# Kernel tuning notes

Measured on AMD Instinct MI355X. Metric: run time of the kernel, lower is better.

The kernel has to match this reference:

```python
import jax, jax.numpy as jnp
import numpy as np
import math

# ---------- real Clebsch-Gordan coupling tables (computed once, tiny) ----------
def _cg(j1, m1, j2, m2, j3, m3):
    if m1 + m2 != m3 or j3 < abs(j1 - j2) or j3 > j1 + j2:
        return 0.0
    f = math.factorial
    pre = ((2 * j3 + 1) * f(j3 + j1 - j2) * f(j3 - j1 + j2) * f(j1 + j2 - j3) / f(j1 + j2 + j3 + 1)) ** 0.5
    pre *= (f(j3 + m3) * f(j3 - m3) * f(j1 - m1) * f(j1 + m1) * f(j2 - m2) * f(j2 + m2)) ** 0.5
    s = 0.0
    for k in range(0, j1 + j2 - j3 + 1):
        d = (k, j1 + j2 - j3 - k, j1 - m1 - k, j2 + m2 - k, j3 - j2 + m1 + k, j3 - j1 - m2 + k)
        if min(d) < 0:
            continue
        den = 1
        for t in d:
            den *= f(t)
        s += (-1) ** k / den
    return pre * s

def _Q(l):  # complex->real spherical-harmonic change of basis
    Q = np.zeros((2 * l + 1, 2 * l + 1), dtype=complex)
    Q[l, l] = 1.0
    s = 2 ** -0.5
    for m in range(1, l + 1):
        Q[l + m, l + m] = (-1) ** m * s
        Q[l + m, l - m] = s
        Q[l - m, l + m] = -1j * (-1) ** m * s
        Q[l - m, l - m] = 1j * s
    return Q

def _K(l1, l2, l3):  # real coupling tensor [2l3+1, 2l1+1, 2l2+1]
    C = np.zeros((2 * l3 + 1, 2 * l1 + 1, 2 * l2 + 1), dtype=complex)
    for M3 in range(-l3, l3 + 1):
        for M1 in range(-l1, l1 + 1):
            for M2 in range(-l2, l2 + 1):
                C[M3 + l3, M1 + l1, M2 + l2] = _cg(l1, M1, l2, M2, l3, M3)
    K = np.einsum('cC,aA,bB,CAB->cab', _Q(l3).conj(), _Q(l1), _Q(l2), C)
    K = K.imag if np.abs(K.imag).max() > np.abs(K.real).max() else K.real
    return np.asarray(K, dtype=np.float32)

# the 9 'uvu' instructions (in_l, edge_l, out_l) with multiplicities (weight_numel=144)
_PATHS = [(0, 0, 0), (0, 2, 2), (1, 0, 1), (1, 2, 1), (1, 2, 2), (2, 0, 2), (2, 2, 0), (2, 2, 1), (2, 2, 2)]
_KT = [jnp.asarray(_K(*p)) for p in _PATHS]
_MULS = [32, 32, 16, 16, 16, 8, 8, 8, 8]
_SPLITS = np.cumsum(_MULS)[:-1].tolist()
NEI = 8
EPS = 1e-5

def _sh(u):  # component-normalized real SH of unit vectors, l=0..2 (m order -l..l, l=1 -> y,z,x)
    x, y, z = u[:, 0], u[:, 1], u[:, 2]
    sh0 = jnp.ones_like(x)[:, None]
    sh1 = np.float32(3 ** 0.5) * jnp.stack([y, z, x], -1)
    s15 = np.float32(15 ** 0.5)
    s5 = np.float32(5 ** 0.5)
    sh2 = jnp.stack([s15 * x * y, s15 * y * z, 0.5 * s5 * (3 * z * z - 1.0), s15 * x * z, 0.5 * s15 * (x * x - y * y)], -1)
    return sh0, sh1, sh2

def _path(xs, sh, wp, Kt):  # xs [E,u,2l1+1], sh [E,2l2+1], Kt [2l3+1,2l1+1,2l2+1] -> [E,u,2l3+1]
    return jnp.einsum('eui,ej,oij->euo', xs, sh, Kt) * wp[None, :, None]

def _layer(x0, x1, x2, pos, src, dst, w, W0, W1, W2, bw0, bb0, bw1, bw2, N):
    ev = pos[dst] - pos[src]
    u = ev / (jnp.linalg.norm(ev, axis=1, keepdims=True) + 1e-12)
    sh0, sh1, sh2 = _sh(u)
    s0 = x0[src][:, :, None]  # [E,32,1]
    s1 = x1[src]              # [E,16,3]
    s2 = x2[src]              # [E,8,5]
    ws = jnp.split(w, _SPLITS)
    p1 = _path(s0, sh0, ws[0], _KT[0])
    p2 = _path(s0, sh2, ws[1], _KT[1])
    p3 = _path(s1, sh0, ws[2], _KT[2])
    p4 = _path(s1, sh2, ws[3], _KT[3])
    p5 = _path(s1, sh2, ws[4], _KT[4])
    p6 = _path(s2, sh0, ws[5], _KT[5])
    p7 = _path(s2, sh2, ws[6], _KT[6])
    p8 = _path(s2, sh2, ws[7], _KT[7])
    p9 = _path(s2, sh2, ws[8], _KT[8])
    m0 = jnp.concatenate([p1, p7], 1)          # [E,40,1]
    m1 = jnp.concatenate([p3, p4, p8], 1)      # [E,40,3]
    m2 = jnp.concatenate([p2, p5, p6, p9], 1)  # [E,64,5]
    a0 = jax.ops.segment_sum(m0, dst, num_segments=N)
    a1 = jax.ops.segment_sum(m1, dst, num_segments=N)
    a2 = jax.ops.segment_sum(m2, dst, num_segments=N)
    y0 = (a0[:, :, 0] @ W0) * np.float32(1.0 / 40 ** 0.5)
    y1 = jnp.einsum('num,uv->nvm', a1, W1) * np.float32(1.0 / 40 ** 0.5)
    y2 = jnp.einsum('num,uv->nvm', a2, W2) * np.float32(1.0 / 64 ** 0.5)
    # equivariant batchnorm (training stats): scalars -> standard BN, l>0 -> norm BN
    f = y0 - y0.mean(0)
    y0 = f / jnp.sqrt((f * f).mean(0) + EPS) * bw0 + bb0
    y1 = y1 / jnp.sqrt((y1 * y1).mean(axis=(0, 2)) + EPS)[None, :, None] * bw1[None, :, None]
    y2 = y2 / jnp.sqrt((y2 * y2).mean(axis=(0, 2)) + EPS)[None, :, None] * bw2[None, :, None]
    return y0, y1, y2

def _forward(positions, W_emb, tp_w, lin_W0, lin_W1, lin_W2, bn_w0, bn_b0, bn_w1, bn_w2, Wf1, Wf2, bf2, Wf3, bf3):
    B, P, _ = positions.shape
    N = B * P
    pos = positions.reshape(N, 3)
    # kNN graph from dense cdist + topk (indices are not differentiated)
    pg = jax.lax.stop_gradient(pos)
    sq = jnp.sum(pg * pg, 1)
    d2 = sq[:, None] + sq[None, :] - 2.0 * (pg @ pg.T)
    _, idx = jax.lax.top_k(-d2, NEI + 1)  # smallest distances; col 0 is self
    src = jnp.repeat(jnp.arange(N), NEI)
    dst = idx[:, 1:].reshape(-1)
    x0 = jnp.ones((N, 1), jnp.float32) @ W_emb  # embedding: only 0e->0e path exists
    x1 = jnp.zeros((N, 16, 3), jnp.float32)
    x2 = jnp.zeros((N, 8, 5), jnp.float32)
    for l in range(3):
        y0, y1, y2 = _layer(x0, x1, x2, pos, src, dst, tp_w[l], lin_W0[l], lin_W1[l], lin_W2[l],
                            bn_w0[l], bn_b0[l], bn_w1[l], bn_w2[l], N)
        x0 = jax.nn.relu(y0) + x0
        x1 = jax.nn.relu(y1) + x1
        x2 = jax.nn.relu(y2) + x2
    h = jax.nn.relu((x0 @ Wf1) * np.float32(1.0 / 32 ** 0.5))  # scalar part -> 32x0e
    h = jax.nn.relu(h @ Wf2 + bf2)
    out = (h @ Wf3 + bf3).reshape(B, P, 2)
    return out

def setup_inputs() -> dict:
    key = jax.random.key(0)
    ks = jax.random.split(key, 16)
    B, P = 4, 2048
    return {
        'positions': jax.random.normal(ks[0], (B, P, 3), jnp.float32) * 3.0,
        'W_emb': jax.random.normal(ks[1], (1, 32), jnp.float32),
        'tp_w': jax.random.normal(ks[2], (3, 144), jnp.float32),
        'lin_W0': jax.random.normal(ks[3], (3, 40, 32), jnp.float32),
        'lin_W1': jax.random.normal(ks[4], (3, 40, 16), jnp.float32),
        'lin_W2': jax.random.normal(ks[5], (3, 64, 8), jnp.float32),
        'bn_w0': 1.0 + 0.05 * jax.random.normal(ks[6], (3, 32), jnp.float32),
        'bn_b0': jnp.zeros((3, 32), jnp.float32),
        'bn_w1': 1.0 + 0.05 * jax.random.normal(ks[7], (3, 16), jnp.float32),
        'bn_w2': 1.0 + 0.05 * jax.random.normal(ks[8], (3, 8), jnp.float32),
        'Wf1': jax.random.normal(ks[9], (32, 32), jnp.float32),
        'Wf2': jax.random.normal(ks[10], (32, 16), jnp.float32) * 0.2,
        'bf2': jax.random.normal(ks[11], (16,), jnp.float32) * 0.1,
        'Wf3': jax.random.normal(ks[12], (16, 2), jnp.float32) * 0.2,
        'bf3': jax.random.normal(ks[13], (2,), jnp.float32) * 0.1,
    }

def reference(positions, W_emb, tp_w, lin_W0, lin_W1, lin_W2, bn_w0, bn_b0, bn_w1, bn_w2, Wf1, Wf2, bf2, Wf3, bf3):
    return _forward(positions, W_emb, tp_w, lin_W0, lin_W1, lin_W2, bn_w0, bn_b0, bn_w1, bn_w2, Wf1, Wf2, bf2, Wf3, bf3)
```

## Files before the change

kernel.cpp:

```cpp
#include <hip/hip_runtime.h>
#include <math.h>

#define NN 8192
#define REV_CAP 48
#define KNN_CAP 512

static const size_t OFF_K     = 0;
static const size_t OFF_CNT   = 512;
static const size_t OFF_REV   = 8704;
static const size_t OFF_STATS = 401920;
static const size_t OFF_XF    = 406528;
static const size_t OFF_YF    = 1389568;
static const size_t WS_FLOATS = 2372608;

__device__ double dfact(int n){ double r=1.0; for(int i=2;i<=n;++i) r*=(double)i; return r; }

__device__ double dcg(int j1,int m1,int j2,int m2,int j3,int m3){
  if (m1+m2!=m3) return 0.0;
  if (j3 < abs(j1-j2) || j3 > j1+j2) return 0.0;
  double pre = sqrt((double)(2*j3+1)*dfact(j3+j1-j2)*dfact(j3-j1+j2)*dfact(j1+j2-j3)/dfact(j1+j2+j3+1));
  pre *= sqrt(dfact(j3+m3)*dfact(j3-m3)*dfact(j1-m1)*dfact(j1+m1)*dfact(j2-m2)*dfact(j2+m2));
  double s=0.0;
  for(int k=0;k<=j1+j2-j3;++k){
    int d1=j1+j2-j3-k, d2=j1-m1-k, d3=j2+m2-k, d4=j3-j2+m1+k, d5=j3-j1-m2+k;
    if(d1<0||d2<0||d3<0||d4<0||d5<0) continue;
    double den = dfact(k)*dfact(d1)*dfact(d2)*dfact(d3)*dfact(d4)*dfact(d5);
    s += ((k&1)? -1.0: 1.0)/den;
  }
  return pre*s;
}

__device__ int qrow(int l,int r,int* col,double* re,double* im){
  const double s = 0.70710678118654752440;
  if (r==l){ col[0]=l; re[0]=1.0; im[0]=0.0; return 1; }
  if (r>l){ int m=r-l;
    col[0]=l+m; re[0]=((m&1)?-s:s); im[0]=0.0;
    col[1]=l-m; re[1]=s;            im[1]=0.0;
  } else { int m=l-r;
    col[0]=l+m; re[0]=0.0; im[0]=((m&1)? s : -s);
    col[1]=l-m; re[1]=0.0; im[1]=s;
  }
  return 2;
}

__global__ __launch_bounds__(256) void k_setup(const float* __restrict__ pos,
        const float* __restrict__ W_emb, float* __restrict__ Kbuf,
        float* __restrict__ xf,
        float* __restrict__ xs, float* __restrict__ ys, float* __restrict__ zs,
        float* __restrict__ qs,
        int* __restrict__ cnt){
  int idx = blockIdx.x*256 + threadIdx.x;
  if (idx < 983040) { const int c = idx%120; xf[idx] = (c<32)? W_emb[c] : 0.f; return; }
  idx -= 983040;
  if (idx < 8192) {
    const float x=pos[3*idx], y=pos[3*idx+1], z=pos[3*idx+2];
    xs[idx]=x; ys[idx]=y; zs[idx]=z; qs[idx]=0.5f*(x*x+y*y+z*z);
    return;
  }
  idx -= 8192;
  if (idx < 8192) { cnt[idx]=0; return; }
  idx -= 8192;
  if (idx >= 405) return;

  const int tid = idx;
  const int sizes[9]={1,25,9,45,75,25,25,75,125};
  const int l1s[9]={0,0,1,1,1,2,2,2,2};
  const int l2s[9]={0,2,0,2,2,0,2,2,2};
  const int l3s[9]={0,2,1,1,2,2,0,1,2};
  int p=0, rem=tid;
  for(p=0;p<9;++p){ if(rem < sizes[p]) break; rem -= sizes[p]; }
  const int l1=l1s[p], l2=l2s[p], l3=l3s[p];
  const int n1=2*l1+1, n2=2*l2+1;
  const int c = rem/(n1*n2); const int r2 = rem%(n1*n2); const int a=r2/n2; const int b=r2%n2;

  int c3[2],c1[2],c2[2]; double re3[2],im3[2],re1[2],im1[2],re2[2],im2[2];
  const int nc3 = qrow(l3,c,c3,re3,im3);
  const int nc1 = qrow(l1,a,c1,re1,im1);
  const int nc2 = qrow(l2,b,c2,re2,im2);

  double accRe=0, accIm=0;
  for(int i3=0;i3<nc3;++i3){
    const double q3re=re3[i3], q3im=-im3[i3];
    for(int i1=0;i1<nc1;++i1){
      const double pre_re = q3re*re1[i1] - q3im*im1[i1];
      const double pre_im = q3re*im1[i1] + q3im*re1[i1];
      for(int i2=0;i2<nc2;++i2){
        const double cgv = dcg(l1, c1[i1]-l1, l2, c2[i2]-l2, l3, c3[i3]-l3);
        if (cgv==0.0) continue;
        accRe += (pre_re*re2[i2] - pre_im*im2[i2])*cgv;
        accIm += (pre_re*im2[i2] + pre_im*re2[i2])*cgv;
      }
    }
  }
  const bool useImag = ((l1+l2+l3)&1)!=0;
  Kbuf[tid] = (float)(useImag? accIm : accRe);
}

__global__ __launch_bounds__(256) void k_knn4(const float* __restrict__ xs,
                                              const float* __restrict__ ys,
                                              const float* __restrict__ zs,
                                              const float* __restrict__ qs,
                                              int* __restrict__ cnt, int* __restrict__ rev){
  const int lane = threadIdx.x & 63;
  const int w    = threadIdx.x >> 6;
  const int node = blockIdx.x*4 + w;
  __shared__ float sdist[4][KNN_CAP];
  __shared__ int   sidx[4][KNN_CAP];
  __shared__ int   scount[4];
  if (threadIdx.x < 4) scount[threadIdx.x]=0;
  __syncthreads();

  const float px = xs[node], py = ys[node], pz = zs[node];

  float m1 = INFINITY, m2 = INFINITY;
  for(int c=0;c<4;++c){
    const int base = (c*64 + lane)*4;
    const float4 fx = *(const float4*)(xs + base);
    const float4 fy = *(const float4*)(ys + base);
    const float4 fz = *(const float4*)(zs + base);
    const float4 fq = *(const float4*)(qs + base);
    float ss[4];
    ss[0] = fmaf(-px,fx.x, fmaf(-py,fy.x, fmaf(-pz,fz.x, fq.x)));
    ss[1] = fmaf(-px,fx.y, fmaf(-py,fy.y, fmaf(-pz,fz.y, fq.y)));
    ss[2] = fmaf(-px,fx.z, fmaf(-py,fy.z, fmaf(-pz,fz.z, fq.z)));
    ss[3] = fmaf(-px,fx.w, fmaf(-py,fy.w, fmaf(-pz,fz.w, fq.w)));
    #pragma unroll
    for(int q=0;q<4;++q){
      const float hi = fmaxf(m1, ss[q]);
      m1 = fminf(m1, ss[q]);
      m2 = fminf(m2, hi);
    }
  }
  float T = INFINITY;
  for(int r=0;r<9;++r){
    float v = m1; int l = lane;
    #pragma unroll
    for(int s=32;s>0;s>>=1){
      const float ov=__shfl_xor(v,s,64); const int ol=__shfl_xor(l,s,64);
      if (ov<v || (ov==v && ol<l)){ v=ov; l=ol; }
    }
    T = v;
    if (lane==l){ m1=m2; m2=INFINITY; }
  }

  for(int c=0;c<32;++c){
    const int base = (c*64 + lane)*4;
    const float4 fx = *(const float4*)(xs + base);
    const float4 fy = *(const float4*)(ys + base);
    const float4 fz = *(const float4*)(zs + base);
    const float4 fq = *(const float4*)(qs + base);
    float ss[4];
    ss[0] = fmaf(-px,fx.x, fmaf(-py,fy.x, fmaf(-pz,fz.x, fq.x)));
    ss[1] = fmaf(-px,fx.y, fmaf(-py,fy.y, fmaf(-pz,fz.y, fq.y)));
    ss[2] = fmaf(-px,fx.z, fmaf(-py,fy.z, fmaf(-pz,fz.z, fq.z)));
    ss[3] = fmaf(-px,fx.w, fmaf(-py,fy.w, fmaf(-pz,fz.w, fq.w)));
    #pragma unroll
    for(int q=0;q<4;++q){
      if (ss[q] <= T){
        int pos = atomicAdd(&scount[w],1);
        if (pos < KNN_CAP){ sdist[w][pos]=ss[q]; sidx[w][pos]=base+q; }
      }
    }
  }
  __syncthreads();

  int m = scount[w]; if (m > KNN_CAP) m = KNN_CAP;
  float dl[KNN_CAP/64]; int il[KNN_CAP/64];
  #pragma unroll
  for(int k=0;k<KNN_CAP/64;++k){
    const int j = lane + 64*k;
    if (j < m){ dl[k]=sdist[w][j]; il[k]=sidx[w][j]; }
    else      { dl[k]=INFINITY;    il[k]=0x7fffffff; }
  }
  for(int r=0;r<9;++r){
    float bv=dl[0]; int bi=il[0];
    #pragma unroll
    for(int k=1;k<KNN_CAP/64;++k){
      if (dl[k]<bv || (dl[k]==bv && il[k]<bi)){ bv=dl[k]; bi=il[k]; }
    }
    float v=bv; int ix=bi;
    #pragma unroll
    for(int s=32;s>0;s>>=1){
      float ov=__shfl_xor(v,s,64); int oi=__shfl_xor(ix,s,64);
      if (ov<v || (ov==v && oi<ix)){ v=ov; ix=oi; }
    }
    if (ix != node && lane==0){
      int cpos = atomicAdd(&cnt[ix],1);
      if (cpos < REV_CAP) rev[ix*REV_CAP + cpos] = node;
    }
    #pragma unroll
    for(int k=0;k<KNN_CAP/64;++k){
      if (il[k]==ix){ dl[k]=INFINITY; il[k]=0x7fffffff; }
    }
  }
}

__global__ __launch_bounds__(256) void k_msg(
  const float* __restrict__ pos,
  const int* __restrict__ cnt, const int* __restrict__ rev,
  const float* __restrict__ Kbuf,
  const float* __restrict__ xf,
  const float* __restrict__ tpw,
  const float* __restrict__ W0, const float* __restrict__ W1, const float* __restrict__ W2,
  float* __restrict__ yf)
{
  const int t = threadIdx.x;
  const int w = t >> 6;
  const int lane = t & 63;
  const int n = blockIdx.x*4 + w;

  __shared__ float KL[405];
  __shared__ float TW[144];
  __shared__ float momP[4][120];
  __shared__ float momS[4][600];
  __shared__ float aS[4][480];
  for(int q=t;q<405;q+=256) KL[q]=Kbuf[q];
  for(int q=t;q<144;q+=256) TW[q]=tpw[q];
  __syncthreads();

  const int deg0 = cnt[n];
  const int deg = (deg0<REV_CAP)? deg0 : REV_CAP;
  const float pnx=pos[3*n], pny=pos[3*n+1], pnz=pos[3*n+2];
  const int c0 = lane*2;
  float mp0=0.f, mp1=0.f;
  float ms0[5], ms1[5];
  #pragma unroll
  for(int j=0;j<5;++j){ ms0[j]=0.f; ms1[j]=0.f; }
  const float s15 = 3.8729833462f, s5c = 2.2360679775f;
  for(int e=0;e<deg;++e){
    const int i = rev[n*REV_CAP+e];
    const float ex = pnx - pos[3*i], ey = pny - pos[3*i+1], ez = pnz - pos[3*i+2];
    const float rn = sqrtf(ex*ex+ey*ey+ez*ez) + 1e-12f;
    const float ux=ex/rn, uy=ey/rn, uz=ez/rn;
    float sh[5];
    sh[0]=s15*ux*uy; sh[1]=s15*uy*uz; sh[2]=0.5f*s5c*(3.f*uz*uz-1.f);
    sh[3]=s15*ux*uz; sh[4]=0.5f*s15*(ux*ux-uy*uy);
    if (lane<60){
      const float2 f = *(const float2*)(xf + (size_t)i*120 + c0);
      mp0 += f.x; mp1 += f.y;
      ms0[0]+=f.x*sh[0]; ms0[1]+=f.x*sh[1]; ms0[2]+=f.x*sh[2]; ms0[3]+=f.x*sh[3]; ms0[4]+=f.x*sh[4];
      ms1[0]+=f.y*sh[0]; ms1[1]+=f.y*sh[1]; ms1[2]+=f.y*sh[2]; ms1[3]+=f.y*sh[3]; ms1[4]+=f.y*sh[4];
    }
  }
  if (lane<60){
    momP[w][c0]=mp0; momP[w][c0+1]=mp1;
    #pragma unroll
    for(int j=0;j<5;++j){ momS[w][c0*5+j]=ms0[j]; momS[w][(c0+1)*5+j]=ms1[j]; }
  }
  __syncthreads();

  float acc[14];
  #pragma unroll
  for(int k=0;k<14;++k) acc[k]=0.f;

  if (lane<32){
    const int u=lane;
    const float rw0=TW[u], rw1=TW[32+u];
    acc[0] = rw0 * KL[0] * momP[w][u];
    float m0s[5];
    #pragma unroll
    for(int j=0;j<5;++j) m0s[j]=momS[w][u*5+j];
    #pragma unroll
    for(int o=0;o<5;++o){ float g=0.f;
      #pragma unroll
      for(int j=0;j<5;++j) g += KL[1+o*5+j]*m0s[j];
      acc[1+o] = rw1*g; }
  } else if (lane<48){
    const int u=lane-32;
    const float rw0=TW[64+u], rw1=TW[80+u], rw2=TW[96+u];
    float m1p[3], m1s[3][5];
    #pragma unroll
    for(int i=0;i<3;++i){
      m1p[i]=momP[w][32+u*3+i];
      #pragma unroll
      for(int j=0;j<5;++j) m1s[i][j]=momS[w][(32+u*3+i)*5+j];
    }
    #pragma unroll
    for(int o=0;o<3;++o){ float g=0.f;
      #pragma unroll
      for(int i=0;i<3;++i) g += KL[26+o*3+i]*m1p[i];
      acc[o]=rw0*g; }
    #pragma unroll
    for(int o=0;o<3;++o){ float g=0.f;
      #pragma unroll
      for(int i=0;i<3;++i)
        #pragma unroll
        for(int j=0;j<5;++j) g += KL[35+(o*3+i)*5+j]*m1s[i][j];
      acc[3+o]=rw1*g; }
    #pragma unroll
    for(int o=0;o<5;++o){ float g=0.f;
      #pragma unroll
      for(int i=0;i<3;++i)
        #pragma unroll
        for(int j=0;j<5;++j) g += KL[80+(o*3+i)*5+j]*m1s[i][j];
      acc[6+o]=rw2*g; }
  } else if (lane<56){
    const int u=lane-48;
    const float rw0=TW[112+u], rw1=TW[120+u], rw2=TW[128+u], rw3=TW[136+u];
    float m2p[5], m2s[5][5];
    #pragma unroll
    for(int i=0;i<5;++i){
      m2p[i]=momP[w][80+u*5+i];
      #pragma unroll
      for(int j=0;j<5;++j) m2s[i][j]=momS[w][(80+u*5+i)*5+j];
    }
    #pragma unroll
    for(int o=0;o<5;++o){ float g=0.f;
      #pragma unroll
      for(int i=0;i<5;++i) g += KL[155+o*5+i]*m2p[i];
      acc[o]=rw0*g; }
    { float g=0.f;
      #pragma unroll
      for(int i=0;i<5;++i)
        #pragma unroll
        for(int j=0;j<5;++j) g += KL[180+i*5+j]*m2s[i][j];
      acc[5]=rw1*g; }
    #pragma unroll
    for(int o=0;o<3;++o){ float g=0.f;
      #pragma unroll
      for(int i=0;i<5;++i)
        #pragma unroll
        for(int j=0;j<5;++j) g += KL[205+(o*5+i)*5+j]*m2s[i][j];
      acc[6+o]=rw2*g; }
    #pragma unroll
    for(int o=0;o<5;++o){ float g=0.f;
      #pragma unroll
      for(int i=0;i<5;++i)
        #pragma unroll
        for(int j=0;j<5;++j) g += KL[280+(o*5+i)*5+j]*m2s[i][j];
      acc[9+o]=rw3*g; }
  }

  if (lane<32){
    aS[w][lane] = acc[0];
    #pragma unroll
    for(int o=0;o<5;++o) aS[w][160 + lane*5+o] = acc[1+o];
  } else if (lane<48){
    const int uu=lane-32;
    #pragma unroll
    for(int m=0;m<3;++m){ aS[w][40 + uu*3+m] = acc[m]; aS[w][40 + (16+uu)*3+m] = acc[3+m]; }
    #pragma unroll
    for(int o=0;o<5;++o) aS[w][160 + (32+uu)*5+o] = acc[6+o];
  } else if (lane<56){
    const int uu=lane-48;
    aS[w][32+uu] = acc[5];
    #pragma unroll
    for(int m=0;m<3;++m) aS[w][40 + (32+uu)*3+m] = acc[6+m];
    #pragma unroll
    for(int o=0;o<5;++o){ aS[w][160 + (48+uu)*5+o] = acc[o]; aS[w][160 + (56+uu)*5+o] = acc[9+o]; }
  }
  __syncthreads();

  const float inv40 = 0.15811388300841896660f;
  for(int q=lane;q<120;q+=64){
    float out;
    if (q<32){
      float g=0.f;
      for(int uu=0;uu<40;++uu) g += aS[w][uu]*W0[uu*32+q];
      out = g*inv40;
    } else if (q<80){
      const int e=q-32, v=e/3, m=e%3;
      float g=0.f;
      for(int uu=0;uu<40;++uu) g += aS[w][40+uu*3+m]*W1[uu*16+v];
      out = g*inv40;
    } else {
      const int e=q-80, tt=e/5, m=e%5;
      float g=0.f;
      for(int uu=0;uu<64;++uu) g += aS[w][160+uu*5+m]*W2[uu*8+tt];
      out = g*0.125f;
    }
    yf[(size_t)n*120+q] = out;
  }
}

__global__ __launch_bounds__(256) void k_statp(const float* __restrict__ yf,
                                               float* __restrict__ pA, float* __restrict__ pB){
  const int ch = blockIdx.x % 96;
  const int chunk = blockIdx.x / 96;
  const int t = threadIdx.x;
  const int n0 = chunk*1024;
  __shared__ float r1[256], r2[256];
  float a1=0.f, a2=0.f;
  if (ch<32){
    for(int nn=t;nn<1024;nn+=256){ float v=yf[(size_t)(n0+nn)*120+ch]; a1+=v; a2+=v*v; }
  } else if (ch<48){
    const int v_=ch-32;
    for(int nn=t;nn<1024;nn+=256){
      #pragma unroll
      for(int m=0;m<3;++m){ float v=yf[(size_t)(n0+nn)*120+32+v_*3+m]; a2+=v*v; }
    }
  } else {
    const int t_=ch-48;
    for(int nn=t;nn<1024;nn+=256){
      #pragma unroll
      for(int m=0;m<5;++m){ float v=yf[(size_t)(n0+nn)*120+80+t_*5+m]; a2+=v*v; }
    }
  }
  r1[t]=a1; r2[t]=a2; __syncthreads();
  for(int s=128;s>0;s>>=1){ if(t<s){ r1[t]+=r1[t+s]; r2[t]+=r2[t+s]; } __syncthreads(); }
  if(t==0){ pA[ch*8+chunk]=r1[0]; pB[ch*8+chunk]=r2[0]; }
}

__global__ __launch_bounds__(256) void k_norm(const float* __restrict__ yf,
                       const float* __restrict__ pA, const float* __restrict__ pB,
                       const float* __restrict__ bw0,const float* __restrict__ bb0,
                       const float* __restrict__ bw1,const float* __restrict__ bw2,
                       float* __restrict__ xf){
  __shared__ float sc[96], sf[32];
  const int t = threadIdx.x;
  if (t<96){
    float sB=0.f;
    #pragma unroll
    for(int k=0;k<8;++k) sB += pB[t*8+k];
    float scale;
    if (t<32){
      float sA=0.f;
      #pragma unroll
      for(int k=0;k<8;++k) sA += pA[t*8+k];
      const float mean = sA*(1.f/8192.f);
      const float var  = sB*(1.f/8192.f) - mean*mean;
      const float inv  = 1.f/sqrtf(var+1e-5f);
      scale = bw0[t]*inv;
      sf[t] = bb0[t] - mean*scale;
    } else if (t<48){
      scale = bw1[t-32]/sqrtf(sB*(1.f/(8192.f*3.f))+1e-5f);
    } else {
      scale = bw2[t-48]/sqrtf(sB*(1.f/(8192.f*5.f))+1e-5f);
    }
    sc[t]=scale;
  }
  __syncthreads();
  const int idx = blockIdx.x*256 + t;
  if (idx >= NN*120) return;
  const int c = idx%120;
  const int chan = (c<32)? c : ((c<80)? 32+(c-32)/3 : 48+(c-80)/5);
  const float v = yf[idx]*sc[chan] + ((c<32)? sf[c] : 0.f);
  xf[idx] += fmaxf(v,0.f);
}

__global__ __launch_bounds__(256) void k_normmlp(const float* __restrict__ yf,
                                             const float* __restrict__ xf,
                                             const float* __restrict__ pA, const float* __restrict__ pB,
                                             const float* __restrict__ bw0,const float* __restrict__ bb0,
                                             const float* __restrict__ Wf1,const float* __restrict__ Wf2,
                                             const float* __restrict__ bf2,const float* __restrict__ Wf3,
                                             const float* __restrict__ bf3, float* __restrict__ out){
  __shared__ float w1[1024], w2[512], w3[32], b2[16], b3[2], sc0[32], sf0[32];
  const int t=threadIdx.x;
  for(int q=t;q<1024;q+=256) w1[q]=Wf1[q];
  for(int q=t;q<512;q+=256)  w2[q]=Wf2[q];
  if(t<32) w3[t]=Wf3[t];
  if(t<16) b2[t]=bf2[t];
  if(t<2)  b3[t]=bf3[t];
  if(t<32){
    float sA=0.f, sB=0.f;
    #pragma unroll
    for(int k=0;k<8;++k){ sA += pA[t*8+k]; sB += pB[t*8+k]; }
    const float mean = sA*(1.f/8192.f);
    const float var  = sB*(1.f/8192.f) - mean*mean;
    const float inv  = 1.f/sqrtf(var+1e-5f);
    sc0[t] = bw0[t]*inv;
    sf0[t] = bb0[t] - mean*sc0[t];
  }
  __syncthreads();
  const int n = blockIdx.x*256+t;
  if(n>=NN) return;
  float xv[32];
  #pragma unroll
  for(int k=0;k<32;++k){
    const float v = yf[(size_t)n*120+k]*sc0[k] + sf0[k];
    xv[k] = xf[(size_t)n*120+k] + fmaxf(v,0.f);
  }
  const float inv32 = 0.17677669529663688110f;
  float h1[32];
  #pragma unroll 4
  for(int c=0;c<32;++c){ float g=0.f;
    #pragma unroll
    for(int k=0;k<32;++k) g+=xv[k]*w1[k*32+c];
    h1[c]=fmaxf(g*inv32,0.f); }
  float h2[16];
  #pragma unroll 4
  for(int c=0;c<16;++c){ float g=b2[c];
    #pragma unroll
    for(int k=0;k<32;++k) g+=h1[k]*w2[k*16+c];
    h2[c]=fmaxf(g,0.f); }
  #pragma unroll
  for(int m=0;m<2;++m){ float g=b3[m];
    #pragma unroll
    for(int k=0;k<16;++k) g+=h2[k]*w3[k*2+m];
    out[n*2+m]=g; }
}

extern "C" void kernel_launch(void* const* d_in, const int* in_sizes, int n_in,
                              void* d_out, int out_size, void* d_ws, size_t ws_size,
                              hipStream_t stream) {
  const float* positions = (const float*)d_in[0];
  const float* W_emb  = (const float*)d_in[1];
  const float* tp_w   = (const float*)d_in[2];
  const float* lin_W0 = (const float*)d_in[3];
  const float* lin_W1 = (const float*)d_in[4];
  const float* lin_W2 = (const float*)d_in[5];
  const float* bn_w0  = (const float*)d_in[6];
  const float* bn_b0  = (const float*)d_in[7];
  const float* bn_w1  = (const float*)d_in[8];
  const float* bn_w2  = (const float*)d_in[9];
  const float* Wf1 = (const float*)d_in[10];
  const float* Wf2 = (const float*)d_in[11];
  const float* bf2 = (const float*)d_in[12];
  const float* Wf3 = (const float*)d_in[13];
  const float* bf3 = (const float*)d_in[14];

  if (ws_size < WS_FLOATS*sizeof(float)) return;

  float* ws    = (float*)d_ws;
  float* Kbuf  = ws + OFF_K;
  int*   cnt   = (int*)(ws + OFF_CNT);
  int*   rev   = (int*)(ws + OFF_REV);
  float* stats = ws + OFF_STATS;
  float* xf = ws + OFF_XF;
  float* yf = ws + OFF_YF;

  float* xs = yf;
  float* ysA = yf + NN;
  float* zs = yf + 2*NN;
  float* qs = yf + 3*NN;

  k_setup<<<3906,256,0,stream>>>(positions, W_emb, Kbuf, xf, xs, ysA, zs, qs, cnt);
  k_knn4<<<NN/4,256,0,stream>>>(xs, ysA, zs, qs, cnt, rev);

  for(int l=0;l<3;++l){
    float* pA = stats + l*1536;
    float* pB = pA + 768;
    k_msg<<<NN/4,256,0,stream>>>(positions, cnt, rev, Kbuf, xf,
                              tp_w + l*144, lin_W0 + l*40*32, lin_W1 + l*40*16, lin_W2 + l*64*8,
                              yf);
    k_statp<<<768,256,0,stream>>>(yf, pA, pB);
    if (l<2){
      k_norm<<<(NN*120+255)/256,256,0,stream>>>(yf, pA, pB,
                              bn_w0 + l*32, bn_b0 + l*32, bn_w1 + l*16, bn_w2 + l*8,
                              xf);
    }
  }
  k_normmlp<<<NN/256,256,0,stream>>>(yf, xf, stats + 2*1536, stats + 2*1536 + 768,
                              bn_w0 + 64, bn_b0 + 64,
                              Wf1, Wf2, bf2, Wf3, bf3, (float*)d_out);
}
```

Baseline: 326.4 us.

## Share candidate scans across block queries and precompute edge harmonics in shared memory

In the kNN kernel, each wave now scans only a quarter of the candidate points. It tests every loaded point against all four query nodes of the block, using thresholds and positions shared through LDS, so each point is loaded once per block instead of four times. In the message kernel, edge indices and spherical harmonics are computed once per edge, in parallel across lanes, and staged in shared memory instead of being recomputed serially by every lane. The cost is more shared-memory atomics that collide across waves and extra LDS traffic.

```diff
diff --git a/kernel.cpp b/kernel.cpp
--- a/kernel.cpp
+++ b/kernel.cpp
@@ -96,21 +96,23 @@
   Kbuf[tid] = (float)(useImag? accIm : accRe);
 }
 
-__global__ __launch_bounds__(256) void k_knn4(const float* __restrict__ xs,
+__global__ __launch_bounds__(256) void k_knn5(const float* __restrict__ xs,
                                               const float* __restrict__ ys,
                                               const float* __restrict__ zs,
                                               const float* __restrict__ qs,
                                               int* __restrict__ cnt, int* __restrict__ rev){
   const int lane = threadIdx.x & 63;
   const int w    = threadIdx.x >> 6;
-  const int node = blockIdx.x*4 + w;
+  const int nodeq = blockIdx.x*4 + w;
   __shared__ float sdist[4][KNN_CAP];
   __shared__ int   sidx[4][KNN_CAP];
   __shared__ int   scount[4];
+  __shared__ float Tsh[4];
+  __shared__ float qp[4][3];
   if (threadIdx.x < 4) scount[threadIdx.x]=0;
-  __syncthreads();
-
-  const float px = xs[node], py = ys[node], pz = zs[node];
+
+  const float px = xs[nodeq], py = ys[nodeq], pz = zs[nodeq];
+  if (lane==0){ qp[w][0]=px; qp[w][1]=py; qp[w][2]=pz; }
 
   float m1 = INFINITY, m2 = INFINITY;
   for(int c=0;c<4;++c){
@@ -142,23 +144,33 @@
     T = v;
     if (lane==l){ m1=m2; m2=INFINITY; }
   }
-
-  for(int c=0;c<32;++c){
-    const int base = (c*64 + lane)*4;
+  if (lane==0) Tsh[w]=T;
+  __syncthreads();
+
+  float qpx[4],qpy[4],qpz[4],Tq[4];
+  #pragma unroll
+  for(int q=0;q<4;++q){ qpx[q]=qp[q][0]; qpy[q]=qp[q][1]; qpz[q]=qp[q][2]; Tq[q]=Tsh[q]; }
+
+  for(int c=0;c<8;++c){
+    const int base = w*2048 + (c*64 + lane)*4;
     const float4 fx = *(const float4*)(xs + base);
     const float4 fy = *(const float4*)(ys + base);
     const float4 fz = *(const float4*)(zs + base);
     const float4 fq = *(const float4*)(qs + base);
-    float ss[4];
-    ss[0] = fmaf(-px,fx.x, fmaf(-py,fy.x, fmaf(-pz,fz.x, fq.x)));
-    ss[1] = fmaf(-px,fx.y, fmaf(-py,fy.y, fmaf(-pz,fz.y, fq.y)));
-    ss[2] = fmaf(-px,fx.z, fmaf(-py,fy.z, fmaf(-pz,fz.z, fq.z)));
-    ss[3] = fmaf(-px,fx.w, fmaf(-py,fy.w, fmaf(-pz,fz.w, fq.w)));
-    #pragma unroll
-    for(int q=0;q<4;++q){
-      if (ss[q] <= T){
-        int pos = atomicAdd(&scount[w],1);
-        if (pos < KNN_CAP){ sdist[w][pos]=ss[q]; sidx[w][pos]=base+q; }
+    float cx[4],cy[4],cz[4],cq[4];
+    cx[0]=fx.x; cx[1]=fx.y; cx[2]=fx.z; cx[3]=fx.w;
+    cy[0]=fy.x; cy[1]=fy.y; cy[2]=fy.z; cy[3]=fy.w;
+    cz[0]=fz.x; cz[1]=fz.y; cz[2]=fz.z; cz[3]=fz.w;
+    cq[0]=fq.x; cq[1]=fq.y; cq[2]=fq.z; cq[3]=fq.w;
+    #pragma unroll
+    for(int j=0;j<4;++j){
+      #pragma unroll
+      for(int q=0;q<4;++q){
+        const float ss = fmaf(-qpx[q],cx[j], fmaf(-qpy[q],cy[j], fmaf(-qpz[q],cz[j], cq[j])));
+        if (ss <= Tq[q]){
+          int pos = atomicAdd(&scount[q],1);
+          if (pos < KNN_CAP){ sdist[q][pos]=ss; sidx[q][pos]=base+j; }
+        }
       }
     }
   }
@@ -184,9 +196,9 @@
       float ov=__shfl_xor(v,s,64); int oi=__shfl_xor(ix,s,64);
       if (ov<v || (ov==v && oi<ix)){ v=ov; ix=oi; }
     }
-    if (ix != node && lane==0){
+    if (ix != nodeq && lane==0){
       int cpos = atomicAdd(&cnt[ix],1);
-      if (cpos < REV_CAP) rev[ix*REV_CAP + cpos] = node;
+      if (cpos < REV_CAP) rev[ix*REV_CAP + cpos] = nodeq;
     }
     #pragma unroll
     for(int k=0;k<KNN_CAP/64;++k){
@@ -214,32 +226,43 @@
   __shared__ float momP[4][120];
   __shared__ float momS[4][600];
   __shared__ float aS[4][480];
+  __shared__ int   eIdx[4][REV_CAP];
+  __shared__ float eSh[4][5][REV_CAP];
   for(int q=t;q<405;q+=256) KL[q]=Kbuf[q];
   for(int q=t;q<144;q+=256) TW[q]=tpw[q];
-  __syncthreads();
 
   const int deg0 = cnt[n];
   const int deg = (deg0<REV_CAP)? deg0 : REV_CAP;
   const float pnx=pos[3*n], pny=pos[3*n+1], pnz=pos[3*n+2];
+  const float s15 = 3.8729833462f, s5c = 2.2360679775f;
+  if (lane < deg){
+    const int i = rev[n*REV_CAP+lane];
+    eIdx[w][lane] = i;
+    const float ex = pnx - pos[3*i], ey = pny - pos[3*i+1], ez = pnz - pos[3*i+2];
+    const float rn = sqrtf(ex*ex+ey*ey+ez*ez) + 1e-12f;
+    const float ux=ex/rn, uy=ey/rn, uz=ez/rn;
+    eSh[w][0][lane]=s15*ux*uy;
+    eSh[w][1][lane]=s15*uy*uz;
+    eSh[w][2][lane]=0.5f*s5c*(3.f*uz*uz-1.f);
+    eSh[w][3][lane]=s15*ux*uz;
+    eSh[w][4][lane]=0.5f*s15*(ux*ux-uy*uy);
+  }
+  __syncthreads();
+
   const int c0 = lane*2;
   float mp0=0.f, mp1=0.f;
   float ms0[5], ms1[5];
   #pragma unroll
   for(int j=0;j<5;++j){ ms0[j]=0.f; ms1[j]=0.f; }
-  const float s15 = 3.8729833462f, s5c = 2.2360679775f;
   for(int e=0;e<deg;++e){
-    const int i = rev[n*REV_CAP+e];
-    const float ex = pnx - pos[3*i], ey = pny - pos[3*i+1], ez = pnz - pos[3*i+2];
-    const float rn = sqrtf(ex*ex+ey*ey+ez*ez) + 1e-12f;
-    const float ux=ex/rn, uy=ey/rn, uz=ez/rn;
-    float sh[5];
-    sh[0]=s15*ux*uy; sh[1]=s15*uy*uz; sh[2]=0.5f*s5c*(3.f*uz*uz-1.f);
-    sh[3]=s15*ux*uz; sh[4]=0.5f*s15*(ux*ux-uy*uy);
+    const int i = eIdx[w][e];
+    const float sh0=eSh[w][0][e], sh1=eSh[w][1][e], sh2=eSh[w][2][e];
+    const float sh3=eSh[w][3][e], sh4=eSh[w][4][e];
     if (lane<60){
       const float2 f = *(const float2*)(xf + (size_t)i*120 + c0);
       mp0 += f.x; mp1 += f.y;
-      ms0[0]+=f.x*sh[0]; ms0[1]+=f.x*sh[1]; ms0[2]+=f.x*sh[2]; ms0[3]+=f.x*sh[3]; ms0[4]+=f.x*sh[4];
-      ms1[0]+=f.y*sh[0]; ms1[1]+=f.y*sh[1]; ms1[2]+=f.y*sh[2]; ms1[3]+=f.y*sh[3]; ms1[4]+=f.y*sh[4];
+      ms0[0]+=f.x*sh0; ms0[1]+=f.x*sh1; ms0[2]+=f.x*sh2; ms0[3]+=f.x*sh3; ms0[4]+=f.x*sh4;
+      ms1[0]+=f.y*sh0; ms1[1]+=f.y*sh1; ms1[2]+=f.y*sh2; ms1[3]+=f.y*sh3; ms1[4]+=f.y*sh4;
     }
   }
   if (lane<60){
@@ -526,7 +549,7 @@
   float* qs = yf + 3*NN;
 
   k_setup<<<3906,256,0,stream>>>(positions, W_emb, Kbuf, xf, xs, ysA, zs, qs, cnt);
-  k_knn4<<<NN/4,256,0,stream>>>(xs, ysA, zs, qs, cnt, rev);
+  k_knn5<<<NN/4,256,0,stream>>>(xs, ysA, zs, qs, cnt, rev);
 
   for(int l=0;l<3;++l){
     float* pA = stats + l*1536;
```

Measured after the change: 309.9 us. 5.1% less time.

## Precompute edge harmonics in parallel and batch neighbor feature gathers in message kernel

Applied to the files above, without the earlier changes.

In the message kernel, each lane now computes one incoming edge's neighbor index and spherical harmonics up front and stores them in shared memory. The first 12 neighbor feature rows are then loaded together into registers before accumulation, so their gather latencies overlap instead of running one after another. Separately, the kNN pre-pass scans twice as many sample points to estimate its distance threshold, and the candidate buffer is halved. This risks overflowing the candidate buffer if the threshold admits more points, and it raises register pressure from the prefetched loads.

```diff
diff --git a/kernel.cpp b/kernel.cpp
--- a/kernel.cpp
+++ b/kernel.cpp
@@ -3,7 +3,8 @@
 
 #define NN 8192
 #define REV_CAP 48
-#define KNN_CAP 512
+#define KNN_CAP 256
+#define PF 12
 
 static const size_t OFF_K     = 0;
 static const size_t OFF_CNT   = 512;
@@ -96,7 +97,7 @@
   Kbuf[tid] = (float)(useImag? accIm : accRe);
 }
 
-__global__ __launch_bounds__(256) void k_knn4(const float* __restrict__ xs,
+__global__ __launch_bounds__(256) void k_knn7(const float* __restrict__ xs,
                                               const float* __restrict__ ys,
                                               const float* __restrict__ zs,
                                               const float* __restrict__ qs,
@@ -113,7 +114,7 @@
   const float px = xs[node], py = ys[node], pz = zs[node];
 
   float m1 = INFINITY, m2 = INFINITY;
-  for(int c=0;c<4;++c){
+  for(int c=0;c<8;++c){
     const int base = (c*64 + lane)*4;
     const float4 fx = *(const float4*)(xs + base);
     const float4 fy = *(const float4*)(ys + base);
@@ -214,32 +215,65 @@
   __shared__ float momP[4][120];
   __shared__ float momS[4][600];
   __shared__ float aS[4][480];
+  __shared__ int   eIdx[4][REV_CAP];
+  __shared__ float eSh[4][5][REV_CAP];
   for(int q=t;q<405;q+=256) KL[q]=Kbuf[q];
   for(int q=t;q<144;q+=256) TW[q]=tpw[q];
-  __syncthreads();
 
   const int deg0 = cnt[n];
   const int deg = (deg0<REV_CAP)? deg0 : REV_CAP;
   const float pnx=pos[3*n], pny=pos[3*n+1], pnz=pos[3*n+2];
+  const float s15 = 3.8729833462f, s5c = 2.2360679775f;
+  if (lane < deg){
+    const int i = rev[n*REV_CAP+lane];
+    eIdx[w][lane] = i;
+    const float ex = pnx - pos[3*i], ey = pny - pos[3*i+1], ez = pnz - pos[3*i+2];
+    const float rn = sqrtf(ex*ex+ey*ey+ez*ez) + 1e-12f;
+    const float ux=ex/rn, uy=ey/rn, uz=ez/rn;
+    eSh[w][0][lane]=s15*ux*uy;
+    eSh[w][1][lane]=s15*uy*uz;
+    eSh[w][2][lane]=0.5f*s5c*(3.f*uz*uz-1.f);
+    eSh[w][3][lane]=s15*ux*uz;
+    eSh[w][4][lane]=0.5f*s15*(ux*ux-uy*uy);
+  }
+  __syncthreads();
+
   const int c0 = lane*2;
   float mp0=0.f, mp1=0.f;
   float ms0[5], ms1[5];
   #pragma unroll
   for(int j=0;j<5;++j){ ms0[j]=0.f; ms1[j]=0.f; }
-  const float s15 = 3.8729833462f, s5c = 2.2360679775f;
-  for(int e=0;e<deg;++e){
-    const int i = rev[n*REV_CAP+e];
-    const float ex = pnx - pos[3*i], ey = pny - pos[3*i+1], ez = pnz - pos[3*i+2];
-    const float rn = sqrtf(ex*ex+ey*ey+ez*ez) + 1e-12f;
-    const float ux=ex/rn, uy=ey/rn, uz=ez/rn;
-    float sh[5];
-    sh[0]=s15*ux*uy; sh[1]=s15*uy*uz; sh[2]=0.5f*s5c*(3.f*uz*uz-1.f);
-    sh[3]=s15*ux*uz; sh[4]=0.5f*s15*(ux*ux-uy*uy);
+
+  int idxr[PF];
+  #pragma unroll
+  for(int k=0;k<PF;++k) idxr[k] = (k<deg)? eIdx[w][k] : 0;
+  float2 fr[PF];
+  if (lane<60){
+    #pragma unroll
+    for(int k=0;k<PF;++k) fr[k] = *(const float2*)(xf + (size_t)idxr[k]*120 + c0);
+  }
+  #pragma unroll
+  for(int k=0;k<PF;++k){
+    if (k<deg){
+      const float sh0=eSh[w][0][k], sh1=eSh[w][1][k], sh2=eSh[w][2][k];
+      const float sh3=eSh[w][3][k], sh4=eSh[w][4][k];
+      if (lane<60){
+        const float2 f = fr[k];
+        mp0 += f.x; mp1 += f.y;
+        ms0[0]+=f.x*sh0; ms0[1]+=f.x*sh1; ms0[2]+=f.x*sh2; ms0[3]+=f.x*sh3; ms0[4]+=f.x*sh4;
+        ms1[0]+=f.y*sh0; ms1[1]+=f.y*sh1; ms1[2]+=f.y*sh2; ms1[3]+=f.y*sh3; ms1[4]+=f.y*sh4;
+      }
+    }
+  }
+  for(int e=PF;e<deg;++e){
+    const int i = eIdx[w][e];
+    const float sh0=eSh[w][0][e], sh1=eSh[w][1][e], sh2=eSh[w][2][e];
+    const float sh3=eSh[w][3][e], sh4=eSh[w][4][e];
     if (lane<60){
       const float2 f = *(const float2*)(xf + (size_t)i*120 + c0);
       mp0 += f.x; mp1 += f.y;
-      ms0[0]+=f.x*sh[0]; ms0[1]+=f.x*sh[1]; ms0[2]+=f.x*sh[2]; ms0[3]+=f.x*sh[3]; ms0[4]+=f.x*sh[4];
-      ms1[0]+=f.y*sh[0]; ms1[1]+=f.y*sh[1]; ms1[2]+=f.y*sh[2]; ms1[3]+=f.y*sh[3]; ms1[4]+=f.y*sh[4];
+      ms0[0]+=f.x*sh0; ms0[1]+=f.x*sh1; ms0[2]+=f.x*sh2; ms0[3]+=f.x*sh3; ms0[4]+=f.x*sh4;
+      ms1[0]+=f.y*sh0; ms1[1]+=f.y*sh1; ms1[2]+=f.y*sh2; ms1[3]+=f.y*sh3; ms1[4]+=f.y*sh4;
     }
   }
   if (lane<60){
@@ -526,7 +560,7 @@
   float* qs = yf + 3*NN;
 
   k_setup<<<3906,256,0,stream>>>(positions, W_emb, Kbuf, xf, xs, ysA, zs, qs, cnt);
-  k_knn4<<<NN/4,256,0,stream>>>(xs, ysA, zs, qs, cnt, rev);
+  k_knn7<<<NN/4,256,0,stream>>>(xs, ysA, zs, qs, cnt, rev);
 
   for(int l=0;l<3;++l){
     float* pA = stats + l*1536;
```

After: 310.0 us. -5.0%, faster.
